# Kernel tuning notes

Hardware: AMD Instinct MI355X
Metric: run time of the kernel (lower is better)

## Reference

```python
import jax, jax.numpy as jnp
import numpy as np

NEG_BIG = 1e9  # large-negative bias used by the original TF code


def setup_inputs() -> dict:
    key = jax.random.key(0)
    kq, kk, kv = jax.random.split(key, 3)
    B, H, W, C, CV = 8, 64, 64, 128, 128
    return {
        "query": jax.random.normal(kq, (B, H, W, C), dtype=jnp.float32),
        "key": jax.random.normal(kk, (B, H, W, C), dtype=jnp.float32),
        "value": jax.random.normal(kv, (B, H, W, CV), dtype=jnp.float32),
    }


def reference(query, key, value):
    B, Hh, Ww, C = query.shape
    CV = value.shape[-1]
    Nq = Hh * Ww                      # canvas_size_q (flattened spatial)
    Nk = key.shape[1] * key.shape[2]  # canvas_size
    q = query.reshape(B, Nq, C)
    k = key.reshape(B, Nk, C)
    v = value.reshape(B, Nk, CV)
    # dense QK^T scores over the flattened canvas: [B, Nq, Nk]
    dot = jnp.einsum('bqc,bkc->bqk', q, k) / jnp.sqrt(jnp.asarray(C, dtype=q.dtype))
    # causal mask: 1 where key position j <= query position i (allowed)
    allowed = jnp.tril(jnp.ones((Nq, Nk), dtype=q.dtype))
    # softmax with large-negative bias on disallowed positions, then re-mask
    probs = jax.nn.softmax(dot - NEG_BIG * (1.0 - allowed), axis=-1) * allowed
    mixed = jnp.einsum('bqk,bkc->bqc', probs, v)
    return mixed.reshape(B, Hh, Ww, CV)
```

## Files before the change

### kernel.cpp

```cpp
#include <hip/hip_runtime.h>
#include <hip/hip_bf16.h>

typedef __bf16 bf16_t;
typedef __attribute__((ext_vector_type(8))) __bf16 bf16x8;
typedef __attribute__((ext_vector_type(4))) __bf16 bf16x4;
typedef __attribute__((ext_vector_type(4))) float floatx4;

static constexpr int NSEQ = 4096;
static constexpr int DIM  = 128;
static constexpr int BATCH = 8;
static constexpr size_t NELEM = (size_t)BATCH * NSEQ * DIM;
static constexpr size_t WS_NEED = 2 * NELEM * sizeof(bf16_t);

static constexpr int CHUNK_T = 16;
static constexpr int NSLOT   = 160;
static constexpr size_t PART_FLOATS = (size_t)BATCH * NSLOT * 64 * 128;
static constexpr size_t LSUM_FLOATS = (size_t)BATCH * NSLOT * 64;
static constexpr size_t WS_SPLITK =
    WS_NEED + (PART_FLOATS + LSUM_FLOATS) * sizeof(float);

static constexpr float SCALE_LOG2E = 0.08838834764831845f * 1.4426950408889634f;

__device__ __forceinline__ int slot_base(int qt) {
  int g = qt >> 4, r = qt & 15;
  return qt + 8 * g * (g - 1) + r * g;
}

__device__ __forceinline__ void gld16(bf16_t* l, const bf16_t* g) {
  __builtin_amdgcn_global_load_lds(
      (const __attribute__((address_space(1))) unsigned int*)g,
      (__attribute__((address_space(3))) unsigned int*)l, 16, 0, 0);
}

__device__ __forceinline__ bf16x8 ld8_f32s(const float* p, float s) {
  float4 a = *(const float4*)p;
  float4 b = *(const float4*)(p + 4);
  bf16x8 r = {(__bf16)(a.x * s), (__bf16)(a.y * s), (__bf16)(a.z * s), (__bf16)(a.w * s),
              (__bf16)(b.x * s), (__bf16)(b.y * s), (__bf16)(b.z * s), (__bf16)(b.w * s)};
  return r;
}


__global__ __launch_bounds__(256)
void prep_kernel(const float* __restrict__ K, const float* __restrict__ V,
                 bf16_t* __restrict__ Kb, bf16_t* __restrict__ Vt) {
  const int bid = blockIdx.x;
  if (bid < 1536) {
    const size_t n4 = NELEM / 4;
    for (size_t i = (size_t)bid * 256 + threadIdx.x; i < n4; i += (size_t)1536 * 256) {
      float4 k = ((const float4*)K)[i];
      bf16x4 kv = {(__bf16)k.x, (__bf16)k.y, (__bf16)k.z, (__bf16)k.w};
      ((bf16x4*)Kb)[i] = kv;
    }
  } else {
    const int id = bid - 1536;
    const int b  = id & 7;
    const int kt = id >> 3;
    const int d4 = (int)threadIdx.x & 31;
    const int kg = (int)threadIdx.x >> 5;
    const float* src = V + ((size_t)(b * NSEQ + kt * 64 + kg * 8) * DIM) + d4 * 4;
    bf16x8 o0, o1, o2, o3;
    #pragma unroll
    for (int j = 0; j < 8; ++j) {
      float4 v = *(const float4*)(src + (size_t)j * DIM);
      o0[j] = (__bf16)v.x; o1[j] = (__bf16)v.y;
      o2[j] = (__bf16)v.z; o3[j] = (__bf16)v.w;
    }
    bf16_t* dst = Vt + ((size_t)b * DIM + d4 * 4) * NSEQ + kt * 64 + kg * 8;
    *(bf16x8*)(dst)            = o0;
    *(bf16x8*)(dst + NSEQ)     = o1;
    *(bf16x8*)(dst + 2 * NSEQ) = o2;
    *(bf16x8*)(dst + 3 * NSEQ) = o3;
  }
}


template <bool MASK>
__device__ __forceinline__ void tile_compute(
    const bf16_t* __restrict__ kbuf, const bf16_t* __restrict__ vbuf,
    bf16_t* __restrict__ pl, const bf16x8 (&qf)[4],
    int l16, int quad, int wq, floatx4 (&acc)[8], float (&lsum)[4]) {
  floatx4 s[4];
  #pragma unroll
  for (int c4 = 0; c4 < 4; ++c4) s[c4] = (floatx4){0.f, 0.f, 0.f, 0.f};
  #pragma unroll
  for (int c4 = 0; c4 < 4; ++c4) {
    const bf16_t* krow = kbuf + (c4 * 16 + l16) * DIM;
    #pragma unroll
    for (int d = 0; d < 4; ++d) {
      bf16x8 kf = *(const bf16x8*)(krow + (((4 * d + quad) ^ l16) * 8));
      s[c4] = __builtin_amdgcn_mfma_f32_16x16x32_bf16(qf[d], kf, s[c4], 0, 0, 0);
    }
  }
  #pragma unroll
  for (int c4 = 0; c4 < 4; ++c4) {
    #pragma unroll
    for (int r = 0; r < 4; ++r) {
      float v = s[c4][r];
      if constexpr (MASK)
        v = (c4 * 16 + l16 <= wq + quad * 4 + r) ? v : -3.0e38f;
      float p = __builtin_amdgcn_exp2f(v);
      lsum[r] += p;
      pl[(quad * 4 + r) * 72 + c4 * 16 + l16] = (__bf16)p;
    }
  }
  asm volatile("s_waitcnt lgkmcnt(0)" ::: "memory");
  bf16x8 pfA = *(const bf16x8*)(pl + l16 * 72 + quad * 8);
  bf16x8 pfB = *(const bf16x8*)(pl + l16 * 72 + 32 + quad * 8);
  #pragma unroll
  for (int c = 0; c < 8; ++c) {
    const bf16_t* vrow = vbuf + (c * 16 + l16) * 64;
    bf16x8 vfA = *(const bf16x8*)(vrow + ((quad ^ (l16 & 7)) * 8));
    bf16x8 vfB = *(const bf16x8*)(vrow + (((quad + 4) ^ (l16 & 7)) * 8));
    acc[c] = __builtin_amdgcn_mfma_f32_16x16x32_bf16(pfA, vfA, acc[c], 0, 0, 0);
    acc[c] = __builtin_amdgcn_mfma_f32_16x16x32_bf16(pfB, vfB, acc[c], 0, 0, 0);
  }
}


__global__ __launch_bounds__(256)
void causal_attn_splitk(const float* __restrict__ Qf, const bf16_t* __restrict__ Kb,
                        const bf16_t* __restrict__ Vt, float* __restrict__ Out,
                        float* __restrict__ Pp, float* __restrict__ Ls) {
  __shared__ __align__(16) bf16_t Kbuf[64 * DIM];
  __shared__ __align__(16) bf16_t Vbuf[DIM * 64];
  __shared__ __align__(16) bf16_t Pbuf[4][16 * 72];

  const int b = (int)blockIdx.x & 7;
  int s = (NSLOT - 1) - ((int)blockIdx.x >> 3);
  int qt = 63, cch = 0;
  {
    int acc0 = 0;
    for (int t = 0; t < 64; ++t) {
      int nch = (t >> 4) + 1;
      if (s < acc0 + nch) { qt = t; cch = s - acc0; break; }
      acc0 += nch;
    }
  }
  const int  nchq   = (qt >> 4) + 1;
  const int  t0     = cch * CHUNK_T;
  const int  nts    = min(CHUNK_T, qt + 1 - t0);
  const bool isLast = (cch == nchq - 1);

  const int tid  = (int)threadIdx.x;
  const int wave = tid >> 6;
  const int lane = tid & 63;
  const int l16  = lane & 15;
  const int quad = lane >> 4;
  const int wq   = wave * 16;

  bf16x8 qf[4];
  {
    const float* qrow = Qf + ((size_t)b * NSEQ + qt * 64 + wq + l16) * DIM + quad * 8;
    #pragma unroll
    for (int d = 0; d < 4; ++d) qf[d] = ld8_f32s(qrow + 32 * d, SCALE_LOG2E);
  }

  const bf16_t* kg0 = Kb + ((size_t)b * NSEQ + 16 * wave) * DIM;
  const bf16_t* vg0 = Vt + ((size_t)b * DIM + 32 * wave) * NSEQ;
  int koff[4], voff[4];
  #pragma unroll
  for (int i = 0; i < 4; ++i) {
    const int krow = 4 * i + (lane >> 4);
    koff[i] = krow * DIM + (((lane & 15) ^ (krow & 15)) * 8);
    const int vrow = 8 * i + (lane >> 3);
    voff[i] = vrow * NSEQ + (((lane & 7) ^ ((lane >> 3) & 7)) * 8);
  }
  bf16_t* kl = Kbuf + 16 * wave * DIM;
  bf16_t* vl = Vbuf + 32 * wave * 64;
  bf16_t* pl = Pbuf[wave];

  floatx4 acc[8];
  #pragma unroll
  for (int c = 0; c < 8; ++c) acc[c] = (floatx4){0.f, 0.f, 0.f, 0.f};
  float lsum[4] = {0.f, 0.f, 0.f, 0.f};

  const int nfull = nts - (isLast ? 1 : 0);
  for (int kt = 0; kt < nfull; ++kt) {
    const int kb = (t0 + kt) * 64;
    #pragma unroll
    for (int i = 0; i < 4; ++i) gld16(kl + i * 512, kg0 + (size_t)kb * DIM + koff[i]);
    #pragma unroll
    for (int i = 0; i < 4; ++i) gld16(vl + i * 512, vg0 + kb + voff[i]);
    __syncthreads();
    tile_compute<false>(Kbuf, Vbuf, pl, qf, l16, quad, wq, acc, lsum);
    __syncthreads();
  }
  if (isLast) {
    const int kb = qt * 64;
    #pragma unroll
    for (int i = 0; i < 4; ++i) gld16(kl + i * 512, kg0 + (size_t)kb * DIM + koff[i]);
    #pragma unroll
    for (int i = 0; i < 4; ++i) gld16(vl + i * 512, vg0 + kb + voff[i]);
    __syncthreads();
    tile_compute<true>(Kbuf, Vbuf, pl, qf, l16, quad, wq, acc, lsum);
  }

  float lred[4];
  #pragma unroll
  for (int r = 0; r < 4; ++r) {
    float s2 = lsum[r];
    #pragma unroll
    for (int off = 1; off < 16; off <<= 1) s2 += __shfl_xor(s2, off, 64);
    lred[r] = s2;
  }

  if (nchq == 1) {
    float* orow = Out + ((size_t)b * NSEQ + qt * 64 + wq + quad * 4) * DIM + l16;
    #pragma unroll
    for (int c = 0; c < 8; ++c) {
      #pragma unroll
      for (int r = 0; r < 4; ++r)
        orow[(size_t)r * DIM + c * 16] = acc[c][r] * (1.0f / lred[r]);
    }
  } else {
    const int slot = b * NSLOT + slot_base(qt) + cch;
    float* pb = Pp + (size_t)slot * (64 * 128) + ((size_t)(wq + quad * 4)) * 128 + l16;
    #pragma unroll
    for (int c = 0; c < 8; ++c) {
      #pragma unroll
      for (int r = 0; r < 4; ++r)
        pb[(size_t)r * 128 + c * 16] = acc[c][r];
    }
    if (l16 == 0) {
      #pragma unroll
      for (int r = 0; r < 4; ++r)
        Ls[(size_t)slot * 64 + wq + quad * 4 + r] = lred[r];
    }
  }
}


__global__ __launch_bounds__(256)
void combine_kernel(const float* __restrict__ Pp, const float* __restrict__ Ls,
                    float* __restrict__ Out) {
  const int e  = (int)blockIdx.x;
  const int b  = e & 7;
  const int qt = 16 + (e >> 3);
  const int s0 = b * NSLOT + slot_base(qt);
  const int nch = (qt >> 4) + 1;
  const int t = (int)threadIdx.x;
  #pragma unroll
  for (int j = 0; j < 8; ++j) {
    const int idx = j * 256 + t;
    const int q   = idx >> 5;
    const int d4  = idx & 31;
    float4 v = {0.f, 0.f, 0.f, 0.f};
    float  l = 0.f;
    for (int ch = 0; ch < nch; ++ch) {
      const float* pc = Pp + (size_t)(s0 + ch) * 8192 + (size_t)q * 128 + d4 * 4;
      float4 a = *(const float4*)pc;
      v.x += a.x; v.y += a.y; v.z += a.z; v.w += a.w;
      l += Ls[(size_t)(s0 + ch) * 64 + q];
    }
    const float inv = 1.0f / l;
    float4 r = {v.x * inv, v.y * inv, v.z * inv, v.w * inv};
    *(float4*)(Out + ((size_t)b * NSEQ + qt * 64 + q) * DIM + d4 * 4) = r;
  }
}


__global__ __launch_bounds__(256)
void causal_attn_kernel(const float* __restrict__ Qf, const bf16_t* __restrict__ Kb,
                        const bf16_t* __restrict__ Vt, float* __restrict__ Out) {
  __shared__ __align__(16) bf16_t Kbuf[64 * DIM];
  __shared__ __align__(16) bf16_t Vbuf[DIM * 64];
  __shared__ __align__(16) bf16_t Pbuf[4][16 * 72];

  const int half = blockIdx.x >> 8;
  const int idx  = blockIdx.x & 255;
  const int b    = idx & 7;
  const int q32  = idx >> 3;
  const int qt64 = half ? q32 : 63 - q32;

  const int tid  = (int)threadIdx.x;
  const int wave = tid >> 6;
  const int lane = tid & 63;
  const int l16  = lane & 15;
  const int quad = lane >> 4;
  const int wq   = wave * 16;

  bf16x8 qf[4];
  {
    const float* qrow = Qf + ((size_t)b * NSEQ + qt64 * 64 + wq + l16) * DIM + quad * 8;
    #pragma unroll
    for (int d = 0; d < 4; ++d) qf[d] = ld8_f32s(qrow + 32 * d, SCALE_LOG2E);
  }

  const bf16_t* kg0 = Kb + ((size_t)b * NSEQ + 16 * wave) * DIM;
  const bf16_t* vg0 = Vt + ((size_t)b * DIM + 32 * wave) * NSEQ;
  int koff[4], voff[4];
  #pragma unroll
  for (int i = 0; i < 4; ++i) {
    const int krow = 4 * i + (lane >> 4);
    koff[i] = krow * DIM + (((lane & 15) ^ (krow & 15)) * 8);
    const int vrow = 8 * i + (lane >> 3);
    voff[i] = vrow * NSEQ + (((lane & 7) ^ ((lane >> 3) & 7)) * 8);
  }
  bf16_t* kl = Kbuf + 16 * wave * DIM;
  bf16_t* vl = Vbuf + 32 * wave * 64;
  bf16_t* pl = Pbuf[wave];

  floatx4 acc[8];
  #pragma unroll
  for (int c = 0; c < 8; ++c) acc[c] = (floatx4){0.f, 0.f, 0.f, 0.f};
  float lsum[4] = {0.f, 0.f, 0.f, 0.f};

  const int nk = qt64 + 1;
  for (int kt = 0; kt < nk - 1; ++kt) {
    const int kb = kt * 64;
    #pragma unroll
    for (int i = 0; i < 4; ++i) gld16(kl + i * 512, kg0 + (size_t)kb * DIM + koff[i]);
    #pragma unroll
    for (int i = 0; i < 4; ++i) gld16(vl + i * 512, vg0 + kb + voff[i]);
    __syncthreads();
    tile_compute<false>(Kbuf, Vbuf, pl, qf, l16, quad, wq, acc, lsum);
    __syncthreads();
  }
  {
    const int kb = (nk - 1) * 64;
    #pragma unroll
    for (int i = 0; i < 4; ++i) gld16(kl + i * 512, kg0 + (size_t)kb * DIM + koff[i]);
    #pragma unroll
    for (int i = 0; i < 4; ++i) gld16(vl + i * 512, vg0 + kb + voff[i]);
    __syncthreads();
    tile_compute<true>(Kbuf, Vbuf, pl, qf, l16, quad, wq, acc, lsum);
  }

  float inv_l[4];
  #pragma unroll
  for (int r = 0; r < 4; ++r) {
    float s = lsum[r];
    #pragma unroll
    for (int off = 1; off < 16; off <<= 1) s += __shfl_xor(s, off, 64);
    inv_l[r] = 1.0f / s;
  }
  float* orow = Out + ((size_t)b * NSEQ + qt64 * 64 + wq + quad * 4) * DIM + l16;
  #pragma unroll
  for (int c = 0; c < 8; ++c) {
    #pragma unroll
    for (int r = 0; r < 4; ++r)
      orow[(size_t)r * DIM + c * 16] = acc[c][r] * inv_l[r];
  }
}


__global__ __launch_bounds__(256)
void causal_attn_fb(const float* __restrict__ Qf, const float* __restrict__ Kf,
                    const float* __restrict__ Vf, float* __restrict__ Out) {
  __shared__ bf16_t p_lds[4][16 * 72];
  const int bid = blockIdx.x, t = bid >> 3, b = bid & 7;
  const int tid = (int)threadIdx.x, wave = tid >> 6, lane = tid & 63;
  const int l16 = lane & 15, quad = lane >> 4;
  const int qtile = (wave < 2) ? t : (127 - t);
  const int q_base = qtile * 32 + (wave & 1) * 16;

  bf16x8 qf[4];
  const float* qrow = Qf + ((size_t)b * NSEQ + q_base + l16) * DIM + quad * 8;
  #pragma unroll
  for (int d = 0; d < 4; ++d) qf[d] = ld8_f32s(qrow + 32 * d, SCALE_LOG2E);

  floatx4 acc[8];
  #pragma unroll
  for (int c = 0; c < 8; ++c) acc[c] = (floatx4){0.f, 0.f, 0.f, 0.f};
  float lsum[4] = {0.f, 0.f, 0.f, 0.f};
  bf16_t* pl = p_lds[wave];
  const int ntiles = (q_base + 16 + 63) >> 6;

  for (int kt = 0; kt < ntiles; ++kt) {
    const int kb = kt * 64;
    floatx4 s[4];
    #pragma unroll
    for (int c4 = 0; c4 < 4; ++c4) s[c4] = (floatx4){0.f, 0.f, 0.f, 0.f};
    const float* kbase = Kf + ((size_t)b * NSEQ + kb + l16) * DIM + quad * 8;
    #pragma unroll
    for (int c4 = 0; c4 < 4; ++c4) {
      #pragma unroll
      for (int d = 0; d < 4; ++d) {
        bf16x8 kf = ld8_f32s(kbase + (size_t)c4 * 16 * DIM + 32 * d, 1.0f);
        s[c4] = __builtin_amdgcn_mfma_f32_16x16x32_bf16(qf[d], kf, s[c4], 0, 0, 0);
      }
    }
    #pragma unroll
    for (int c4 = 0; c4 < 4; ++c4) {
      #pragma unroll
      for (int r = 0; r < 4; ++r) {
        float v = s[c4][r];
        const int qi = q_base + quad * 4 + r;
        v = (kb + c4 * 16 + l16 <= qi) ? v : -3.0e38f;
        float p = __builtin_amdgcn_exp2f(v);
        lsum[r] += p;
        pl[(quad * 4 + r) * 72 + c4 * 16 + l16] = (__bf16)p;
      }
    }
    asm volatile("s_waitcnt lgkmcnt(0)" ::: "memory");
    bf16x8 pfA = *(const bf16x8*)(pl + l16 * 72 + quad * 8);
    bf16x8 pfB = *(const bf16x8*)(pl + l16 * 72 + 32 + quad * 8);
    const float* vb = Vf + ((size_t)b * NSEQ + kb) * DIM;
    #pragma unroll
    for (int c = 0; c < 8; ++c) {
      bf16x8 vfA, vfB;
      #pragma unroll
      for (int j = 0; j < 8; ++j) {
        vfA[j] = (__bf16)vb[(size_t)(quad * 8 + j) * DIM + c * 16 + l16];
        vfB[j] = (__bf16)vb[(size_t)(32 + quad * 8 + j) * DIM + c * 16 + l16];
      }
      acc[c] = __builtin_amdgcn_mfma_f32_16x16x32_bf16(pfA, vfA, acc[c], 0, 0, 0);
      acc[c] = __builtin_amdgcn_mfma_f32_16x16x32_bf16(pfB, vfB, acc[c], 0, 0, 0);
    }
  }
  float inv_l[4];
  #pragma unroll
  for (int r = 0; r < 4; ++r) {
    float s = lsum[r];
    #pragma unroll
    for (int off = 1; off < 16; off <<= 1) s += __shfl_xor(s, off, 64);
    inv_l[r] = 1.0f / s;
  }
  float* orow = Out + ((size_t)b * NSEQ + q_base + quad * 4) * DIM + l16;
  #pragma unroll
  for (int c = 0; c < 8; ++c) {
    #pragma unroll
    for (int r = 0; r < 4; ++r)
      orow[(size_t)r * DIM + c * 16] = acc[c][r] * inv_l[r];
  }
}

extern "C" void kernel_launch(void* const* d_in, const int* in_sizes, int n_in,
                              void* d_out, int out_size, void* d_ws, size_t ws_size,
                              hipStream_t stream) {
  const float* Q = (const float*)d_in[0];
  const float* K = (const float*)d_in[1];
  const float* V = (const float*)d_in[2];
  float* Out = (float*)d_out;
  (void)in_sizes; (void)n_in; (void)out_size;

  dim3 block(256);
  if (ws_size >= WS_SPLITK) {
    bf16_t* Kb = (bf16_t*)d_ws;
    bf16_t* Vt = Kb + NELEM;
    float*  Pp = (float*)((char*)d_ws + WS_NEED);
    float*  Ls = Pp + PART_FLOATS;
    prep_kernel<<<dim3(2048), block, 0, stream>>>(K, V, Kb, Vt);
    causal_attn_splitk<<<dim3(BATCH * NSLOT), block, 0, stream>>>(Q, Kb, Vt, Out, Pp, Ls);
    combine_kernel<<<dim3(BATCH * 48), block, 0, stream>>>(Pp, Ls, Out);
  } else if (ws_size >= WS_NEED) {
    bf16_t* Kb = (bf16_t*)d_ws;
    bf16_t* Vt = Kb + NELEM;
    prep_kernel<<<dim3(2048), block, 0, stream>>>(K, V, Kb, Vt);
    causal_attn_kernel<<<dim3(512), block, 0, stream>>>(Q, Kb, Vt, Out);
  } else {
    causal_attn_fb<<<dim3(512), block, 0, stream>>>(Q, K, V, Out);
  }
}
```

Baseline: 172.9 us.

## Use 128-row query tiles with strided split-K chunks and LDS-staged V transpose

The split-K attention kernel now processes 128 query rows per block: each wave handles two 16-row MFMA tiles that share every K/V fragment read from LDS. This halves K/V reloads per query row. Key tiles are assigned to chunks in an interleaved stride, and the slot map, workspace layout and combine kernel change to match, with a choice between fine and coarse chunking based on workspace size. The V transpose in prep now goes through an LDS tile, MFMA sections are wrapped in setprio, and launch bounds request 3 blocks per CU. Costs are higher register pressure and larger partial buffers, plus a possible fallback if the workspace is too small for the new sizes.

```diff
diff --git a/kernel.cpp b/kernel.cpp
--- a/kernel.cpp
+++ b/kernel.cpp
@@ -12,18 +12,18 @@
 static constexpr size_t NELEM = (size_t)BATCH * NSEQ * DIM;
 static constexpr size_t WS_NEED = 2 * NELEM * sizeof(bf16_t);
 
-static constexpr int CHUNK_T = 16;
-static constexpr int NSLOT   = 160;
-static constexpr size_t PART_FLOATS = (size_t)BATCH * NSLOT * 64 * 128;
-static constexpr size_t LSUM_FLOATS = (size_t)BATCH * NSLOT * 64;
-static constexpr size_t WS_SPLITK =
-    WS_NEED + (PART_FLOATS + LSUM_FLOATS) * sizeof(float);
+static constexpr int NSLOT_C = 80;
+static constexpr int NSLOT_F = 144;
+static constexpr size_t WS_COARSE =
+    WS_NEED + (size_t)BATCH * NSLOT_C * (16384 + 128) * sizeof(float);
+static constexpr size_t WS_FINE =
+    WS_NEED + (size_t)BATCH * NSLOT_F * (16384 + 128) * sizeof(float);
 
 static constexpr float SCALE_LOG2E = 0.08838834764831845f * 1.4426950408889634f;
 
-__device__ __forceinline__ int slot_base(int qt) {
-  int g = qt >> 4, r = qt & 15;
-  return qt + 8 * g * (g - 1) + r * g;
+__device__ __forceinline__ int slot_base_d(int qt, int lb) {
+  int g = qt >> lb, r = qt & ((1 << lb) - 1);
+  return (1 << lb) * ((g * (g + 1)) >> 1) + r * (g + 1);
 }
 
 __device__ __forceinline__ void gld16(bf16_t* l, const bf16_t* g) {
@@ -44,6 +44,7 @@
 __global__ __launch_bounds__(256)
 void prep_kernel(const float* __restrict__ K, const float* __restrict__ V,
                  bf16_t* __restrict__ Kb, bf16_t* __restrict__ Vt) {
+  __shared__ bf16_t ldsT[128 * 66];
   const int bid = blockIdx.x;
   if (bid < 1536) {
     const size_t n4 = NELEM / 4;
@@ -56,21 +57,248 @@
     const int id = bid - 1536;
     const int b  = id & 7;
     const int kt = id >> 3;
-    const int d4 = (int)threadIdx.x & 31;
-    const int kg = (int)threadIdx.x >> 5;
-    const float* src = V + ((size_t)(b * NSEQ + kt * 64 + kg * 8) * DIM) + d4 * 4;
-    bf16x8 o0, o1, o2, o3;
-    #pragma unroll
-    for (int j = 0; j < 8; ++j) {
-      float4 v = *(const float4*)(src + (size_t)j * DIM);
-      o0[j] = (__bf16)v.x; o1[j] = (__bf16)v.y;
-      o2[j] = (__bf16)v.z; o3[j] = (__bf16)v.w;
-    }
-    bf16_t* dst = Vt + ((size_t)b * DIM + d4 * 4) * NSEQ + kt * 64 + kg * 8;
-    *(bf16x8*)(dst)            = o0;
-    *(bf16x8*)(dst + NSEQ)     = o1;
-    *(bf16x8*)(dst + 2 * NSEQ) = o2;
-    *(bf16x8*)(dst + 3 * NSEQ) = o3;
+    const float* src = V + ((size_t)(b * NSEQ + kt * 64)) * DIM;
+    #pragma unroll
+    for (int it = 0; it < 8; ++it) {
+      const int idx = it * 256 + (int)threadIdx.x;
+      const int k = idx >> 5, c4 = idx & 31;
+      float4 v = ((const float4*)src)[idx];
+      ldsT[(c4 * 4 + 0) * 66 + k] = (__bf16)v.x;
+      ldsT[(c4 * 4 + 1) * 66 + k] = (__bf16)v.y;
+      ldsT[(c4 * 4 + 2) * 66 + k] = (__bf16)v.z;
+      ldsT[(c4 * 4 + 3) * 66 + k] = (__bf16)v.w;
+    }
+    __syncthreads();
+    #pragma unroll
+    for (int it = 0; it < 4; ++it) {
+      const int task = it * 256 + (int)threadIdx.x;
+      const int d = task >> 3, kg = task & 7;
+      bf16x8 o;
+      #pragma unroll
+      for (int j = 0; j < 8; ++j) o[j] = ldsT[d * 66 + kg * 8 + j];
+      *(bf16x8*)(Vt + ((size_t)b * DIM + d) * NSEQ + kt * 64 + kg * 8) = o;
+    }
+  }
+}
+
+
+template <bool MASK>
+__device__ __forceinline__ void tile_compute2(
+    const bf16_t* __restrict__ kbuf, const bf16_t* __restrict__ vbuf,
+    bf16_t* __restrict__ pl, const bf16x8 (&qf)[2][4],
+    int l16, int quad, int wq32, int dd,
+    floatx4 (&acc)[2][8], float (&lsum)[2][4]) {
+  #pragma unroll
+  for (int c4 = 0; c4 < 4; ++c4) {
+    floatx4 s0 = {0.f, 0.f, 0.f, 0.f}, s1 = {0.f, 0.f, 0.f, 0.f};
+    const bf16_t* krow = kbuf + (c4 * 16 + l16) * DIM;
+    #pragma unroll
+    for (int d = 0; d < 4; ++d) {
+      bf16x8 kf = *(const bf16x8*)(krow + (((4 * d + quad) ^ l16) * 8));
+      s0 = __builtin_amdgcn_mfma_f32_16x16x32_bf16(qf[0][d], kf, s0, 0, 0, 0);
+      s1 = __builtin_amdgcn_mfma_f32_16x16x32_bf16(qf[1][d], kf, s1, 0, 0, 0);
+    }
+    #pragma unroll
+    for (int r = 0; r < 4; ++r) {
+      float v0 = s0[r], v1 = s1[r];
+      if constexpr (MASK) {
+        const int key = dd + c4 * 16 + l16;
+        v0 = (key <= wq32 + quad * 4 + r) ? v0 : -3.0e38f;
+        v1 = (key <= wq32 + 16 + quad * 4 + r) ? v1 : -3.0e38f;
+      }
+      float p0 = __builtin_amdgcn_exp2f(v0);
+      float p1 = __builtin_amdgcn_exp2f(v1);
+      lsum[0][r] += p0; lsum[1][r] += p1;
+      pl[(quad * 4 + r) * 72 + c4 * 16 + l16] = (__bf16)p0;
+      pl[(16 + quad * 4 + r) * 72 + c4 * 16 + l16] = (__bf16)p1;
+    }
+  }
+  asm volatile("s_waitcnt lgkmcnt(0)" ::: "memory");
+  bf16x8 pfA0 = *(const bf16x8*)(pl + l16 * 72 + quad * 8);
+  bf16x8 pfB0 = *(const bf16x8*)(pl + l16 * 72 + 32 + quad * 8);
+  bf16x8 pfA1 = *(const bf16x8*)(pl + (16 + l16) * 72 + quad * 8);
+  bf16x8 pfB1 = *(const bf16x8*)(pl + (16 + l16) * 72 + 32 + quad * 8);
+  __builtin_amdgcn_s_setprio(1);
+  #pragma unroll
+  for (int c = 0; c < 8; ++c) {
+    const bf16_t* vrow = vbuf + (c * 16 + l16) * 64;
+    bf16x8 vfA = *(const bf16x8*)(vrow + ((quad ^ (l16 & 7)) * 8));
+    bf16x8 vfB = *(const bf16x8*)(vrow + (((quad + 4) ^ (l16 & 7)) * 8));
+    acc[0][c] = __builtin_amdgcn_mfma_f32_16x16x32_bf16(pfA0, vfA, acc[0][c], 0, 0, 0);
+    acc[0][c] = __builtin_amdgcn_mfma_f32_16x16x32_bf16(pfB0, vfB, acc[0][c], 0, 0, 0);
+    acc[1][c] = __builtin_amdgcn_mfma_f32_16x16x32_bf16(pfA1, vfA, acc[1][c], 0, 0, 0);
+    acc[1][c] = __builtin_amdgcn_mfma_f32_16x16x32_bf16(pfB1, vfB, acc[1][c], 0, 0, 0);
+  }
+  __builtin_amdgcn_s_setprio(0);
+}
+
+
+__global__ __launch_bounds__(256, 3)
+void causal_attn_splitk(const float* __restrict__ Qf, const bf16_t* __restrict__ Kb,
+                        const bf16_t* __restrict__ Vt, float* __restrict__ Out,
+                        float* __restrict__ Pp, float* __restrict__ Ls,
+                        int lb, int nslot) {
+  __shared__ __align__(16) bf16_t Kbuf[64 * DIM];
+  __shared__ __align__(16) bf16_t Vbuf[DIM * 64];
+  __shared__ __align__(16) bf16_t Pbuf[4][32 * 72];
+
+  const int b = (int)blockIdx.x & 7;
+  const int s = (nslot - 1) - ((int)blockIdx.x >> 3);
+  int qt = 0, cch = 0;
+  {
+    const int bs = 1 << lb;
+    int acc0 = 0;
+    for (int g = 0; g < (32 >> lb); ++g) {
+      const int bandw = bs * (g + 1);
+      if (s < acc0 + bandw) {
+        const int u = s - acc0;
+        qt = g * bs + u / (g + 1);
+        cch = u % (g + 1);
+        break;
+      }
+      acc0 += bandw;
+    }
+  }
+  const int ntot = 2 * qt + 2;
+  const int nch  = (qt >> lb) + 1;
+  const int nt_c = (ntot - 1 - cch) / nch + 1;
+
+  const int tid  = (int)threadIdx.x;
+  const int wave = tid >> 6;
+  const int lane = tid & 63;
+  const int l16  = lane & 15;
+  const int quad = lane >> 4;
+  const int wq32 = wave * 32;
+
+  bf16x8 qf[2][4];
+  #pragma unroll
+  for (int m = 0; m < 2; ++m) {
+    const float* qrow =
+        Qf + ((size_t)b * NSEQ + qt * 128 + wq32 + m * 16 + l16) * DIM + quad * 8;
+    #pragma unroll
+    for (int d = 0; d < 4; ++d) qf[m][d] = ld8_f32s(qrow + 32 * d, SCALE_LOG2E);
+  }
+
+  const bf16_t* kg0 = Kb + ((size_t)b * NSEQ + 16 * wave) * DIM;
+  const bf16_t* vg0 = Vt + ((size_t)b * DIM + 32 * wave) * NSEQ;
+  int koff[4], voff[4];
+  #pragma unroll
+  for (int i = 0; i < 4; ++i) {
+    const int krow = 4 * i + (lane >> 4);
+    koff[i] = krow * DIM + (((lane & 15) ^ (krow & 15)) * 8);
+    const int vrow = 8 * i + (lane >> 3);
+    voff[i] = vrow * NSEQ + (((lane & 7) ^ ((lane >> 3) & 7)) * 8);
+  }
+  bf16_t* kl = Kbuf + 16 * wave * DIM;
+  bf16_t* vl = Vbuf + 32 * wave * 64;
+  bf16_t* pl = Pbuf[wave];
+
+  floatx4 acc[2][8];
+  #pragma unroll
+  for (int m = 0; m < 2; ++m)
+    #pragma unroll
+    for (int c = 0; c < 8; ++c) acc[m][c] = (floatx4){0.f, 0.f, 0.f, 0.f};
+  float lsum[2][4] = {{0.f, 0.f, 0.f, 0.f}, {0.f, 0.f, 0.f, 0.f}};
+
+  int nmask;
+  if (nch == 1) nmask = 2;
+  else nmask = (cch + (nt_c - 1) * nch >= ntot - 2) ? 1 : 0;
+  const int nfull = nt_c - nmask;
+
+  int t = cch;
+  for (int i = 0; i < nfull; ++i, t += nch) {
+    const size_t kb = (size_t)t * 64;
+    #pragma unroll
+    for (int i2 = 0; i2 < 4; ++i2) gld16(kl + i2 * 512, kg0 + kb * DIM + koff[i2]);
+    #pragma unroll
+    for (int i2 = 0; i2 < 4; ++i2) gld16(vl + i2 * 512, vg0 + kb + voff[i2]);
+    __syncthreads();
+    tile_compute2<false>(Kbuf, Vbuf, pl, qf, l16, quad, wq32, 0, acc, lsum);
+    __syncthreads();
+  }
+  for (int i = 0; i < nmask; ++i, t += nch) {
+    const size_t kb = (size_t)t * 64;
+    #pragma unroll
+    for (int i2 = 0; i2 < 4; ++i2) gld16(kl + i2 * 512, kg0 + kb * DIM + koff[i2]);
+    #pragma unroll
+    for (int i2 = 0; i2 < 4; ++i2) gld16(vl + i2 * 512, vg0 + kb + voff[i2]);
+    __syncthreads();
+    const int dd = (t - 2 * qt) * 64;
+    if (dd + 63 <= wq32)
+      tile_compute2<false>(Kbuf, Vbuf, pl, qf, l16, quad, wq32, 0, acc, lsum);
+    else if (wq32 + 31 >= dd)
+      tile_compute2<true>(Kbuf, Vbuf, pl, qf, l16, quad, wq32, dd, acc, lsum);
+    __syncthreads();
+  }
+
+  float lred[2][4];
+  #pragma unroll
+  for (int m = 0; m < 2; ++m)
+    #pragma unroll
+    for (int r = 0; r < 4; ++r) {
+      float s2 = lsum[m][r];
+      #pragma unroll
+      for (int off = 1; off < 16; off <<= 1) s2 += __shfl_xor(s2, off, 64);
+      lred[m][r] = s2;
+    }
+
+  if (nch == 1) {
+    #pragma unroll
+    for (int m = 0; m < 2; ++m) {
+      float* orow =
+          Out + ((size_t)b * NSEQ + qt * 128 + wq32 + m * 16 + quad * 4) * DIM + l16;
+      #pragma unroll
+      for (int c = 0; c < 8; ++c)
+        #pragma unroll
+        for (int r = 0; r < 4; ++r)
+          orow[(size_t)r * DIM + c * 16] = acc[m][c][r] * (1.0f / lred[m][r]);
+    }
+  } else {
+    const int slot = b * nslot + slot_base_d(qt, lb) + cch;
+    #pragma unroll
+    for (int m = 0; m < 2; ++m) {
+      float* pb = Pp + (size_t)slot * 16384 +
+                  ((size_t)(wq32 + m * 16 + quad * 4)) * 128 + l16;
+      #pragma unroll
+      for (int c = 0; c < 8; ++c)
+        #pragma unroll
+        for (int r = 0; r < 4; ++r)
+          pb[(size_t)r * 128 + c * 16] = acc[m][c][r];
+      if (l16 == 0) {
+        #pragma unroll
+        for (int r = 0; r < 4; ++r)
+          Ls[(size_t)slot * 128 + wq32 + m * 16 + quad * 4 + r] = lred[m][r];
+      }
+    }
+  }
+}
+
+
+__global__ __launch_bounds__(256)
+void combine_kernel(const float* __restrict__ Pp, const float* __restrict__ Ls,
+                    float* __restrict__ Out, int lb, int nslot) {
+  const int e  = (int)blockIdx.x;
+  const int b  = e & 7;
+  const int qt = (1 << lb) + (e >> 3);
+  const int s0 = b * nslot + slot_base_d(qt, lb);
+  const int nch = (qt >> lb) + 1;
+  const int t = (int)threadIdx.x;
+  #pragma unroll
+  for (int j = 0; j < 16; ++j) {
+    const int idx = j * 256 + t;
+    const int q   = idx >> 5;
+    const int d4  = idx & 31;
+    float4 v = {0.f, 0.f, 0.f, 0.f};
+    float  l = 0.f;
+    for (int ch = 0; ch < nch; ++ch) {
+      const float* pc = Pp + (size_t)(s0 + ch) * 16384 + (size_t)q * 128 + d4 * 4;
+      float4 a = *(const float4*)pc;
+      v.x += a.x; v.y += a.y; v.z += a.z; v.w += a.w;
+      l += Ls[(size_t)(s0 + ch) * 128 + q];
+    }
+    const float inv = 1.0f / l;
+    float4 r = {v.x * inv, v.y * inv, v.z * inv, v.w * inv};
+    *(float4*)(Out + ((size_t)b * NSEQ + qt * 128 + q) * DIM + d4 * 4) = r;
   }
 }
 
@@ -116,149 +344,6 @@
     acc[c] = __builtin_amdgcn_mfma_f32_16x16x32_bf16(pfB, vfB, acc[c], 0, 0, 0);
   }
 }
-
-
-__global__ __launch_bounds__(256)
-void causal_attn_splitk(const float* __restrict__ Qf, const bf16_t* __restrict__ Kb,
-                        const bf16_t* __restrict__ Vt, float* __restrict__ Out,
-                        float* __restrict__ Pp, float* __restrict__ Ls) {
-  __shared__ __align__(16) bf16_t Kbuf[64 * DIM];
-  __shared__ __align__(16) bf16_t Vbuf[DIM * 64];
-  __shared__ __align__(16) bf16_t Pbuf[4][16 * 72];
-
-  const int b = (int)blockIdx.x & 7;
-  int s = (NSLOT - 1) - ((int)blockIdx.x >> 3);
-  int qt = 63, cch = 0;
-  {
-    int acc0 = 0;
-    for (int t = 0; t < 64; ++t) {
-      int nch = (t >> 4) + 1;
-      if (s < acc0 + nch) { qt = t; cch = s - acc0; break; }
-      acc0 += nch;
-    }
-  }
-  const int  nchq   = (qt >> 4) + 1;
-  const int  t0     = cch * CHUNK_T;
-  const int  nts    = min(CHUNK_T, qt + 1 - t0);
-  const bool isLast = (cch == nchq - 1);
-
-  const int tid  = (int)threadIdx.x;
-  const int wave = tid >> 6;
-  const int lane = tid & 63;
-  const int l16  = lane & 15;
-  const int quad = lane >> 4;
-  const int wq   = wave * 16;
-
-  bf16x8 qf[4];
-  {
-    const float* qrow = Qf + ((size_t)b * NSEQ + qt * 64 + wq + l16) * DIM + quad * 8;
-    #pragma unroll
-    for (int d = 0; d < 4; ++d) qf[d] = ld8_f32s(qrow + 32 * d, SCALE_LOG2E);
-  }
-
-  const bf16_t* kg0 = Kb + ((size_t)b * NSEQ + 16 * wave) * DIM;
-  const bf16_t* vg0 = Vt + ((size_t)b * DIM + 32 * wave) * NSEQ;
-  int koff[4], voff[4];
-  #pragma unroll
-  for (int i = 0; i < 4; ++i) {
-    const int krow = 4 * i + (lane >> 4);
-    koff[i] = krow * DIM + (((lane & 15) ^ (krow & 15)) * 8);
-    const int vrow = 8 * i + (lane >> 3);
-    voff[i] = vrow * NSEQ + (((lane & 7) ^ ((lane >> 3) & 7)) * 8);
-  }
-  bf16_t* kl = Kbuf + 16 * wave * DIM;
-  bf16_t* vl = Vbuf + 32 * wave * 64;
-  bf16_t* pl = Pbuf[wave];
-
-  floatx4 acc[8];
-  #pragma unroll
-  for (int c = 0; c < 8; ++c) acc[c] = (floatx4){0.f, 0.f, 0.f, 0.f};
-  float lsum[4] = {0.f, 0.f, 0.f, 0.f};
-
-  const int nfull = nts - (isLast ? 1 : 0);
-  for (int kt = 0; kt < nfull; ++kt) {
-    const int kb = (t0 + kt) * 64;
-    #pragma unroll
-    for (int i = 0; i < 4; ++i) gld16(kl + i * 512, kg0 + (size_t)kb * DIM + koff[i]);
-    #pragma unroll
-    for (int i = 0; i < 4; ++i) gld16(vl + i * 512, vg0 + kb + voff[i]);
-    __syncthreads();
-    tile_compute<false>(Kbuf, Vbuf, pl, qf, l16, quad, wq, acc, lsum);
-    __syncthreads();
-  }
-  if (isLast) {
-    const int kb = qt * 64;
-    #pragma unroll
-    for (int i = 0; i < 4; ++i) gld16(kl + i * 512, kg0 + (size_t)kb * DIM + koff[i]);
-    #pragma unroll
-    for (int i = 0; i < 4; ++i) gld16(vl + i * 512, vg0 + kb + voff[i]);
-    __syncthreads();
-    tile_compute<true>(Kbuf, Vbuf, pl, qf, l16, quad, wq, acc, lsum);
-  }
-
-  float lred[4];
-  #pragma unroll
-  for (int r = 0; r < 4; ++r) {
-    float s2 = lsum[r];
-    #pragma unroll
-    for (int off = 1; off < 16; off <<= 1) s2 += __shfl_xor(s2, off, 64);
-    lred[r] = s2;
-  }
-
-  if (nchq == 1) {
-    float* orow = Out + ((size_t)b * NSEQ + qt * 64 + wq + quad * 4) * DIM + l16;
-    #pragma unroll
-    for (int c = 0; c < 8; ++c) {
-      #pragma unroll
-      for (int r = 0; r < 4; ++r)
-        orow[(size_t)r * DIM + c * 16] = acc[c][r] * (1.0f / lred[r]);
-    }
-  } else {
-    const int slot = b * NSLOT + slot_base(qt) + cch;
-    float* pb = Pp + (size_t)slot * (64 * 128) + ((size_t)(wq + quad * 4)) * 128 + l16;
-    #pragma unroll
-    for (int c = 0; c < 8; ++c) {
-      #pragma unroll
-      for (int r = 0; r < 4; ++r)
-        pb[(size_t)r * 128 + c * 16] = acc[c][r];
-    }
-    if (l16 == 0) {
-      #pragma unroll
-      for (int r = 0; r < 4; ++r)
-        Ls[(size_t)slot * 64 + wq + quad * 4 + r] = lred[r];
-    }
-  }
-}
-
-
-__global__ __launch_bounds__(256)
-void combine_kernel(const float* __restrict__ Pp, const float* __restrict__ Ls,
-                    float* __restrict__ Out) {
-  const int e  = (int)blockIdx.x;
-  const int b  = e & 7;
-  const int qt = 16 + (e >> 3);
-  const int s0 = b * NSLOT + slot_base(qt);
-  const int nch = (qt >> 4) + 1;
-  const int t = (int)threadIdx.x;
-  #pragma unroll
-  for (int j = 0; j < 8; ++j) {
-    const int idx = j * 256 + t;
-    const int q   = idx >> 5;
-    const int d4  = idx & 31;
-    float4 v = {0.f, 0.f, 0.f, 0.f};
-    float  l = 0.f;
-    for (int ch = 0; ch < nch; ++ch) {
-      const float* pc = Pp + (size_t)(s0 + ch) * 8192 + (size_t)q * 128 + d4 * 4;
-      float4 a = *(const float4*)pc;
-      v.x += a.x; v.y += a.y; v.z += a.z; v.w += a.w;
-      l += Ls[(size_t)(s0 + ch) * 64 + q];
-    }
-    const float inv = 1.0f / l;
-    float4 r = {v.x * inv, v.y * inv, v.z * inv, v.w * inv};
-    *(float4*)(Out + ((size_t)b * NSEQ + qt * 64 + q) * DIM + d4 * 4) = r;
-  }
-}
-
 
 __global__ __launch_bounds__(256)
 void causal_attn_kernel(const float* __restrict__ Qf, const bf16_t* __restrict__ Kb,
@@ -436,14 +521,19 @@
   (void)in_sizes; (void)n_in; (void)out_size;
 
   dim3 block(256);
-  if (ws_size >= WS_SPLITK) {
+  if (ws_size >= WS_COARSE) {
+    const bool fine = (ws_size >= WS_FINE);
+    const int lb = fine ? 2 : 3;
+    const int nslot = fine ? NSLOT_F : NSLOT_C;
     bf16_t* Kb = (bf16_t*)d_ws;
     bf16_t* Vt = Kb + NELEM;
     float*  Pp = (float*)((char*)d_ws + WS_NEED);
-    float*  Ls = Pp + PART_FLOATS;
+    float*  Ls = Pp + (size_t)BATCH * nslot * 16384;
     prep_kernel<<<dim3(2048), block, 0, stream>>>(K, V, Kb, Vt);
-    causal_attn_splitk<<<dim3(BATCH * NSLOT), block, 0, stream>>>(Q, Kb, Vt, Out, Pp, Ls);
-    combine_kernel<<<dim3(BATCH * 48), block, 0, stream>>>(Pp, Ls, Out);
+    causal_attn_splitk<<<dim3(BATCH * nslot), block, 0, stream>>>(Q, Kb, Vt, Out, Pp, Ls,
+                                                                  lb, nslot);
+    combine_kernel<<<dim3(BATCH * (32 - (1 << lb))), block, 0, stream>>>(Pp, Ls, Out,
+                                                                         lb, nslot);
   } else if (ws_size >= WS_NEED) {
     bf16_t* Kb = (bf16_t*)d_ws;
     bf16_t* Vt = Kb + NELEM;
```

Measured after the change: 196.8 us. 1.14x slower.
